# Performance work log

Hardware: AMD Instinct MI355X
Metric: run time of the kernel (lower is better)

The kernel has to match this reference:

```python
import math
import jax, jax.numpy as jnp
import numpy as np

B, L, DM = 2, 1024, 1024
STATE, EXPAND, CONV, DTR = 16, 2, 4, 8
INNER = DM * EXPAND          # 2048
NFFT = L // 2 + 1            # 513


def _silu(v):
    return v * jax.nn.sigmoid(v)


def setup_inputs() -> dict:
    key = jax.random.key(0)
    ks = jax.random.split(key, 12)
    s = lambda k, shape, sc=0.02: (jax.random.normal(k, shape, jnp.float32) * sc)
    # dt_proj bias initialized like the torch module: exp(U(0,1)*(log dt_max - log dt_min) + log dt_min)
    inv_dt = jnp.exp(jax.random.uniform(ks[10], (INNER,), jnp.float32)
                     * (math.log(0.1) - math.log(0.001)) + math.log(0.001))
    return {
        "x": jax.random.normal(ks[0], (B, L, DM), jnp.float32),
        "in_proj_w": s(ks[1], (2 * INNER, DM)),
        "conv_w": s(ks[2], (INNER, 1, CONV), 0.1),      # depthwise conv kernel
        "conv_b": jnp.zeros((INNER,), jnp.float32),
        "A_log": jnp.tile(jnp.log(jnp.arange(1, STATE + 1, dtype=jnp.float32)), (INNER, 1)),
        "D": jnp.ones((INNER,), jnp.float32),
        "x_proj_w": s(ks[3], (DTR + 2 * STATE, INNER)),
        "dt_proj_w": s(ks[4], (INNER, DTR)),
        "dt_proj_b": inv_dt,
        "filter_real": s(ks[5], (INNER, NFFT)),
        "filter_imag": s(ks[6], (INNER, NFFT)),
        "spectral_decay": jnp.ones((INNER,), jnp.float32) * 0.01,
        "fusion_w": s(ks[7], (INNER, 2 * INNER)),
        "fusion_b": jnp.zeros((INNER,), jnp.float32),
        "out_proj_w": s(ks[8], (DM, INNER)),
        "ln_gamma": jnp.ones((DM,), jnp.float32),
        "ln_beta": jnp.zeros((DM,), jnp.float32),
    }


def reference(x, in_proj_w, conv_w, conv_b, A_log, D, x_proj_w, dt_proj_w, dt_proj_b,
              filter_real, filter_imag, spectral_decay, fusion_w, fusion_b,
              out_proj_w, ln_gamma, ln_beta):
    residual = x
    xz = x @ in_proj_w.T                                   # [B,L,2*INNER]
    x_inner, z = xz[..., :INNER], xz[..., INNER:]
    z = _silu(z)

    # ---- SSM path ----
    xc = jnp.swapaxes(x_inner, 1, 2)                       # [B,E,L]
    xc = jax.lax.conv_general_dilated(
        xc, conv_w, (1,), [(CONV - 1, 0)],                 # causal depthwise conv (pad-left == torch pad + truncate)
        dimension_numbers=("NCH", "OIH", "NCH"),
        feature_group_count=INNER) + conv_b[None, :, None]
    x_conv = jnp.swapaxes(_silu(xc), 1, 2)                 # [B,L,E]

    x_dbc = x_conv @ x_proj_w.T                            # [B,L,DTR+2S]
    dt_x = x_dbc[..., :DTR]
    Bm = x_dbc[..., DTR:DTR + STATE]                       # [B,L,S]
    Cm = x_dbc[..., DTR + STATE:]                          # [B,L,S]
    dt = jax.nn.softplus(dt_x @ dt_proj_w.T + dt_proj_b)   # [B,L,E]
    A = -jnp.exp(A_log)                                    # [E,S]
    dA = jnp.exp(dt[..., None] * A)                        # [B,L,E,S]
    dBx = (dt * x_conv)[..., None] * Bm[:, :, None, :]     # [B,L,E,S]

    def step(h, inp):
        dA_t, dBx_t, C_t = inp
        h = dA_t * h + dBx_t                               # [B,E,S]
        return h, jnp.einsum('bes,bs->be', h, C_t)

    h0 = jnp.zeros((B, INNER, STATE), x.dtype)
    _, ys = jax.lax.scan(step, h0,
                         (jnp.swapaxes(dA, 0, 1), jnp.swapaxes(dBx, 0, 1), jnp.swapaxes(Cm, 0, 1)))
    y_ssm = jnp.swapaxes(ys, 0, 1) + x_conv * D            # [B,L,E]

    # ---- Spectral path ----
    xf = jnp.fft.rfft(jnp.swapaxes(x_inner, 1, 2), axis=-1)        # [B,E,NFFT]
    freqs = jnp.linspace(0.0, 1.0, NFFT)
    filt = (filter_real + 1j * filter_imag) * jnp.exp(-spectral_decay[:, None] * freqs[None, :])
    y_spec = jnp.swapaxes(jnp.fft.irfft(xf * filt[None], n=L, axis=-1), 1, 2)  # [B,L,E]

    # ---- Gated fusion ----
    g = jax.nn.sigmoid(jnp.concatenate([y_ssm, y_spec], -1) @ fusion_w.T + fusion_b)
    y = g * y_ssm + (1.0 - g) * y_spec
    y = y * z
    out = y @ out_proj_w.T + residual                      # [B,L,DM]

    mu = out.mean(-1, keepdims=True)
    var = out.var(-1, keepdims=True)
    return (out - mu) / jnp.sqrt(var + 1e-5) * ln_gamma + ln_beta
```

## Files before the change

kernel.cpp:

```cpp
#include <hip/hip_runtime.h>
#include <math.h>

#define B_ 2
#define L_ 1024
#define DM_ 1024
#define STATE_ 16
#define CONV_ 4
#define DTR_ 8
#define INNER_ 2048
#define M_ (B_*L_)
#define MD_ (B_*INNER_)
#define NFFT_ 513
#define NFP_ 1152
#define NCH_ 32
#define CHL_ 32
#define SK_ 32
#define KSL_ (2048/SK_)

typedef unsigned short u16;
typedef __attribute__((ext_vector_type(8))) short short8;
typedef __attribute__((ext_vector_type(8))) __bf16 bf16x8;
typedef __attribute__((ext_vector_type(4))) float f32x4;

__device__ __forceinline__ float frcp_(float x) { return __builtin_amdgcn_rcpf(x); }
__device__ __forceinline__ float fexp_(float x) { return __expf(x); }
__device__ __forceinline__ float fsigm_(float x) { return frcp_(1.f + __expf(-x)); }
__device__ __forceinline__ float fsilu_(float x) { return x * frcp_(1.f + __expf(-x)); }
__device__ __forceinline__ float fsoftplus_(float v) {
  return (v > 20.f) ? v : __logf(1.f + __expf(v));
}
__device__ __forceinline__ u16 f2bf(float f) {
  union { float f; unsigned u; } v; v.f = f;
  unsigned r = v.u + 0x7fffu + ((v.u >> 16) & 1u);
  return (u16)(r >> 16);
}
__device__ __forceinline__ float bf2f(u16 h) {
  union { unsigned u; float f; } v; v.u = ((unsigned)h) << 16;
  return v.f;
}
__device__ __forceinline__ void gload16(const void* g, void* l) {
  __builtin_amdgcn_global_load_lds(
      (const __attribute__((address_space(1))) unsigned*)g,
      (__attribute__((address_space(3))) unsigned*)l, 16, 0, 0);
}
__device__ __forceinline__ f32x4 mfma_bf16(short8 a, short8 b, f32x4 c) {
  return __builtin_amdgcn_mfma_f32_16x16x32_bf16(
      __builtin_bit_cast(bf16x8, a), __builtin_bit_cast(bf16x8, b), c, 0, 0, 0);
}

#define CVT_N0 2097152
#define CVT_N1 6291456
#define CVT_N2 14680064
#define CVT_NT 16777216
__global__ __launch_bounds__(256) void cvt4_k(
    const float* __restrict__ s0, const float* __restrict__ s1,
    const float* __restrict__ s2, const float* __restrict__ s3,
    u16* __restrict__ out)
{
  int i = (blockIdx.x*256 + threadIdx.x) * 4;
  const float* src; int off;
  if (i < CVT_N0)      { src = s0; off = 0; }
  else if (i < CVT_N1) { src = s1; off = CVT_N0; }
  else if (i < CVT_N2) { src = s2; off = CVT_N1; }
  else                 { src = s3; off = CVT_N2; }
  float4 v = *(const float4*)(src + (i - off));
  ushort4 o;
  o.x = f2bf(v.x); o.y = f2bf(v.y); o.z = f2bf(v.z); o.w = f2bf(v.w);
  *(ushort4*)(out + i) = o;
}

template<int TM, int TN, int EPI>
__global__ __launch_bounds__((TM/64)*(TN/32)*64) void mgemm_k(
    const u16* __restrict__ Ab, const u16* __restrict__ Bb,
    void* __restrict__ Cout, int K, int ldc,
    const float* __restrict__ aux0, u16* __restrict__ aux1,
    const float* __restrict__ aux2, const float* __restrict__ aux3)
{
  constexpr int WN   = TN/32;
  constexpr int NW   = (TM/64)*WN;
  constexpr int NTHR = NW*64;
  __shared__ __align__(16) u16 As[2][TM*64];
  __shared__ __align__(16) u16 Bs[2][TN*64];
  const int t = threadIdx.x;
  const int lane = t & 63;
  const int w = t >> 6;
  const int wm = w / WN, wn = w % WN;
  const int M0 = blockIdx.y * TM, N0 = blockIdx.x * TN;

  f32x4 acc[4][2] = {};

  auto stage = [&](int buf, int k0) {
    #pragma unroll
    for (int q = 0; q < TM*8/NTHR; q++) {
      int u = q*NTHR + t;
      int row = u >> 3, gpr = u & 7;
      int grp = gpr ^ (row & 7);
      gload16(Ab + (size_t)(M0+row)*K + k0 + grp*8, &As[buf][u*8]);
    }
    #pragma unroll
    for (int q = 0; q < TN*8/NTHR; q++) {
      int u = q*NTHR + t;
      int row = u >> 3, gpr = u & 7;
      int grp = gpr ^ (row & 7);
      gload16(Bb + (size_t)(N0+row)*K + k0 + grp*8, &Bs[buf][u*8]);
    }
  };

  stage(0, 0);
  const int nk = K >> 6;
  for (int ks = 0; ks < nk; ks++) {
    const int buf = ks & 1;
    __syncthreads();
    if (ks + 1 < nk) stage(buf ^ 1, (ks + 1) << 6);
    const u16* Asb = As[buf];
    const u16* Bsb = Bs[buf];
    #pragma unroll
    for (int kk = 0; kk < 2; kk++) {
      const int quad = lane >> 4;
      const int grp = kk*4 + quad;
      short8 af[4], bf[2];
      #pragma unroll
      for (int i = 0; i < 4; i++) {
        int row = wm*64 + i*16 + (lane & 15);
        af[i] = *(const short8*)&Asb[(row*8 + (grp ^ (row & 7)))*8];
      }
      #pragma unroll
      for (int j = 0; j < 2; j++) {
        int row = wn*32 + j*16 + (lane & 15);
        bf[j] = *(const short8*)&Bsb[(row*8 + (grp ^ (row & 7)))*8];
      }
      #pragma unroll
      for (int i = 0; i < 4; i++)
        #pragma unroll
        for (int j = 0; j < 2; j++)
          acc[i][j] = mfma_bf16(af[i], bf[j], acc[i][j]);
    }
  }

  #pragma unroll
  for (int i = 0; i < 4; i++) {
    int mbase = M0 + wm*64 + i*16 + (lane >> 4)*4;
    #pragma unroll
    for (int j = 0; j < 2; j++) {
      int n = N0 + wn*32 + j*16 + (lane & 15);
      #pragma unroll
      for (int r = 0; r < 4; r++) {
        int m = mbase + r;
        float v = acc[i][j][r];
        if (EPI == 0) {
          ((float*)Cout)[(size_t)m*ldc + n] = v;
        } else if (EPI == 1) {
          float g  = fsigm_(v + aux0[n]);
          float ys = bf2f(aux1[(size_t)m*4096 + n]);
          float yp = bf2f(aux1[(size_t)m*4096 + 2048 + n]);
          float z  = aux2[(size_t)m*4096 + 2048 + n];
          ((u16*)Cout)[(size_t)m*ldc + n] = f2bf((g*ys + (1.f-g)*yp)*fsilu_(z));
        } else if (EPI == 2) {
          ((float*)Cout)[(size_t)m*ldc + n] = v + aux2[(size_t)m*ldc + n];
        } else if (EPI == 3) {
          float pv = __shfl_xor(v, 1, 64);
          int f = n >> 1;
          float outv = 0.f;
          if (f < NFFT_) {
            int c = m & (INNER_-1);
            float d  = fexp_(-aux2[c] * (float)f * (1.f/512.f));
            float wr = aux0[c*NFFT_+f]*d, wi = aux3[c*NFFT_+f]*d;
            float a = (n & 1) ? pv : v;
            float b = (n & 1) ? v : pv;
            outv = (n & 1) ? (a*wi + b*wr) : (a*wr - b*wi);
          }
          ((u16*)Cout)[(size_t)m*ldc + n] = f2bf(outv);
        } else if (EPI == 5) {
          ((float*)Cout)[(size_t)m*ldc + n] = v;
          if (n < 2048) {
            int b2 = m >> 10, l2 = m & 1023;
            aux1[((size_t)(b2*2048 + n) << 10) + l2] = f2bf(v);
          }
        } else {
          int b2 = m >> 11, c2 = m & (INNER_-1);
          ((u16*)Cout)[((size_t)((b2 << 10) + n) << 12) + 2048 + c2] = f2bf(v);
        }
      }
    }
  }
}

__global__ __launch_bounds__(256) void xproj_k(
    const float* __restrict__ xconv, const float* __restrict__ W,
    float* __restrict__ part)
{
  __shared__ float Bs[40][KSL_+4];
  const int sk = blockIdx.x, mt = blockIdx.y;
  const int k0 = sk*KSL_;
  for (int i = threadIdx.x; i < 40*KSL_; i += 256) {
    int n = i >> 6, k = i & (KSL_-1);
    Bs[n][k] = W[(size_t)n*2048 + k0 + k];
  }
  __syncthreads();
  const int m = mt*256 + threadIdx.x;
  const float* arow = xconv + (size_t)m*2048 + k0;
  float acc[40];
  #pragma unroll
  for (int j=0;j<40;j++) acc[j]=0.f;
  for (int k = 0; k < KSL_; k += 4) {
    float4 a = *(const float4*)(arow + k);
    #pragma unroll
    for (int j = 0; j < 40; j++) {
      float4 b = *(const float4*)&Bs[j][k];
      acc[j] += a.x*b.x + a.y*b.y + a.z*b.z + a.w*b.w;
    }
  }
  float* o = part + ((size_t)sk*M_ + m)*40;
  #pragma unroll
  for (int j = 0; j < 10; j++)
    *(float4*)(o + j*4) = make_float4(acc[j*4], acc[j*4+1], acc[j*4+2], acc[j*4+3]);
}

__global__ __launch_bounds__(256) void xpred_k(const float* __restrict__ part,
                                               float* __restrict__ xdbc)
{
  int i = blockIdx.x*256 + threadIdx.x;
  float s = 0.f;
  #pragma unroll
  for (int sk = 0; sk < SK_; sk++) s += part[(size_t)sk*81920 + i];
  xdbc[i] = s;
}

__global__ __launch_bounds__(256) void conv_silu_k(
    const float* __restrict__ xz, const float* __restrict__ cw,
    const float* __restrict__ cb, float* __restrict__ xc)
{
  int idx = blockIdx.x*256 + threadIdx.x;
  int c = idx & (INNER_-1);
  int g = idx >> 11;
  int b = g >> 7;
  int lb = (g & 127) * 8;
  float w0=cw[c*4+0], w1=cw[c*4+1], w2=cw[c*4+2], w3=cw[c*4+3];
  float bias = cb[c];
  float v[11];
  #pragma unroll
  for (int j = 0; j < 11; j++) {
    int l = lb - 3 + j;
    v[j] = (l >= 0) ? xz[((size_t)((b << 10) + l))*4096 + c] : 0.f;
  }
  #pragma unroll
  for (int j = 0; j < 8; j++) {
    float s = bias + w0*v[j] + w1*v[j+1] + w2*v[j+2] + w3*v[j+3];
    xc[((size_t)((b << 10) + lb + j))*INNER_ + c] = fsilu_(s);
  }
}

__global__ __launch_bounds__(256) void scan1_k(
    const float* __restrict__ xdbc, const float* __restrict__ xconv,
    const float* __restrict__ A_log, const float* __restrict__ dtw,
    const float* __restrict__ dtb, float* __restrict__ Pq)
{
  int idx = blockIdx.x*256 + threadIdx.x;
  int e  = idx & (INNER_-1);
  int bc = idx >> 11;
  int ch = bc & (NCH_-1);
  int b  = bc >> 5;
  float A[STATE_];
  #pragma unroll
  for (int s=0;s<STATE_;s++) A[s] = -fexp_(A_log[e*STATE_+s]);
  float w[DTR_];
  #pragma unroll
  for (int r=0;r<DTR_;r++) w[r] = dtw[e*DTR_+r];
  float bias = dtb[e];
  float h[STATE_] = {};
  float sdt = 0.f;
  int mbase = b*L_ + ch*CHL_;
  float dtx[DTR_], Bv[STATE_], xcv;
  {
    const float* row = xdbc + (size_t)mbase*40;
    #pragma unroll
    for (int r=0;r<DTR_;r++) dtx[r] = row[r];
    #pragma unroll
    for (int s=0;s<STATE_;s++) Bv[s] = row[8+s];
    xcv = xconv[(size_t)mbase*INNER_ + e];
  }
  for (int l=0;l<CHL_;l++) {
    float ndtx[DTR_], nBv[STATE_], nxcv = 0.f;
    if (l+1 < CHL_) {
      const float* nrow = xdbc + (size_t)(mbase+l+1)*40;
      #pragma unroll
      for (int r=0;r<DTR_;r++) ndtx[r] = nrow[r];
      #pragma unroll
      for (int s=0;s<STATE_;s++) nBv[s] = nrow[8+s];
      nxcv = xconv[(size_t)(mbase+l+1)*INNER_ + e];
    } else {
      #pragma unroll
      for (int r=0;r<DTR_;r++) ndtx[r] = 0.f;
      #pragma unroll
      for (int s=0;s<STATE_;s++) nBv[s] = 0.f;
    }
    float v = bias;
    #pragma unroll
    for (int r=0;r<DTR_;r++) v += dtx[r]*w[r];
    float dt = fsoftplus_(v);
    sdt += dt;
    float dx = dt * xcv;
    #pragma unroll
    for (int s=0;s<STATE_;s++) {
      float dA = fexp_(dt*A[s]);
      h[s] = dA*h[s] + dx*Bv[s];
    }
    #pragma unroll
    for (int r=0;r<DTR_;r++) dtx[r] = ndtx[r];
    #pragma unroll
    for (int s=0;s<STATE_;s++) Bv[s] = nBv[s];
    xcv = nxcv;
  }
  float* o = Pq + (size_t)idx*32;
  #pragma unroll
  for (int s=0;s<STATE_;s++) { o[s] = fexp_(A[s]*sdt); o[16+s] = h[s]; }
}

__global__ __launch_bounds__(256) void scan2_k(float* __restrict__ Pq)
{
  int idx = blockIdx.x*256 + threadIdx.x;
  int s = idx & 15;
  int e = (idx >> 4) & (INNER_-1);
  int b = idx >> 15;
  float h = 0.f;
  for (int ch = 0; ch < NCH_; ch++) {
    size_t base = ((size_t)(b*NCH_+ch)*INNER_ + e)*32;
    float p = Pq[base + s];
    float q = Pq[base + 16 + s];
    Pq[base + 16 + s] = h;
    h = p*h + q;
  }
}

__global__ __launch_bounds__(256) void scan3_k(
    const float* __restrict__ xdbc, const float* __restrict__ xconv,
    const float* __restrict__ A_log, const float* __restrict__ dtw,
    const float* __restrict__ dtb, const float* __restrict__ Dp,
    const float* __restrict__ Pq, u16* __restrict__ ycat)
{
  int idx = blockIdx.x*256 + threadIdx.x;
  int e  = idx & (INNER_-1);
  int bc = idx >> 11;
  int ch = bc & (NCH_-1);
  int b  = bc >> 5;
  float A[STATE_];
  #pragma unroll
  for (int s=0;s<STATE_;s++) A[s] = -fexp_(A_log[e*STATE_+s]);
  float w[DTR_];
  #pragma unroll
  for (int r=0;r<DTR_;r++) w[r] = dtw[e*DTR_+r];
  float bias = dtb[e];
  float Dv = Dp[e];
  float h[STATE_];
  const float* hi = Pq + (size_t)idx*32 + 16;
  #pragma unroll
  for (int s=0;s<STATE_;s++) h[s] = hi[s];
  int mbase = b*L_ + ch*CHL_;
  float dtx[DTR_], Bv[STATE_], Cv[STATE_], xcv;
  {
    const float* row = xdbc + (size_t)mbase*40;
    #pragma unroll
    for (int r=0;r<DTR_;r++) dtx[r] = row[r];
    #pragma unroll
    for (int s=0;s<STATE_;s++) { Bv[s] = row[8+s]; Cv[s] = row[24+s]; }
    xcv = xconv[(size_t)mbase*INNER_ + e];
  }
  for (int l=0;l<CHL_;l++) {
    float ndtx[DTR_], nBv[STATE_], nCv[STATE_], nxcv = 0.f;
    if (l+1 < CHL_) {
      const float* nrow = xdbc + (size_t)(mbase+l+1)*40;
      #pragma unroll
      for (int r=0;r<DTR_;r++) ndtx[r] = nrow[r];
      #pragma unroll
      for (int s=0;s<STATE_;s++) { nBv[s] = nrow[8+s]; nCv[s] = nrow[24+s]; }
      nxcv = xconv[(size_t)(mbase+l+1)*INNER_ + e];
    } else {
      #pragma unroll
      for (int r=0;r<DTR_;r++) ndtx[r] = 0.f;
      #pragma unroll
      for (int s=0;s<STATE_;s++) { nBv[s] = 0.f; nCv[s] = 0.f; }
    }
    float v = bias;
    #pragma unroll
    for (int r=0;r<DTR_;r++) v += dtx[r]*w[r];
    float dt = fsoftplus_(v);
    float dx = dt * xcv;
    float y = 0.f;
    #pragma unroll
    for (int s=0;s<STATE_;s++) {
      float dA = fexp_(dt*A[s]);
      h[s] = dA*h[s] + dx*Bv[s];
      y += h[s]*Cv[s];
    }
    ycat[(size_t)(mbase+l)*4096 + e] = f2bf(y + xcv*Dv);
    #pragma unroll
    for (int r=0;r<DTR_;r++) dtx[r] = ndtx[r];
    #pragma unroll
    for (int s=0;s<STATE_;s++) { Bv[s] = nBv[s]; Cv[s] = nCv[s]; }
    xcv = nxcv;
  }
}

__global__ __launch_bounds__(256) void genWdftb_k(u16* __restrict__ W) {
  int idx = blockIdx.x*256 + threadIdx.x;
  int l = idx & (L_-1);
  int col = idx >> 10;
  float v = 0.f;
  int f = col >> 1;
  if (f < NFFT_) {
    int ph = (l*f) & (L_-1);
    float th = (float)ph * (6.283185307179586f / (float)L_);
    v = (col & 1) ? -__sinf(th) : __cosf(th);
  }
  W[idx] = f2bf(v);
}

__global__ __launch_bounds__(256) void genWinvb_k(u16* __restrict__ W) {
  int idx = blockIdx.x*256 + threadIdx.x;
  int r = idx % NFP_;
  int l = idx / NFP_;
  int f = r >> 1;
  float v = 0.f;
  if (f < NFFT_) {
    bool edge = (f == 0) || (f == 512);
    float sc = (edge ? 1.f : 2.f) / (float)L_;
    int ph = (f*l) & (L_-1);
    float th = (float)ph * (6.283185307179586f / (float)L_);
    if (r & 1) v = edge ? 0.f : -sc*__sinf(th);
    else       v = sc*__cosf(th);
  }
  W[idx] = f2bf(v);
}

__global__ __launch_bounds__(256) void ln_k(const float* __restrict__ inp,
    const float* __restrict__ gma, const float* __restrict__ bta,
    float* __restrict__ out)
{
  int m = blockIdx.x;
  const float* row = inp + (size_t)m*DM_;
  float s=0.f, s2=0.f;
  float v[4];
  #pragma unroll
  for (int j=0;j<4;j++) {
    v[j] = row[threadIdx.x + j*256];
    s += v[j]; s2 += v[j]*v[j];
  }
  #pragma unroll
  for (int off=32; off>=1; off>>=1) {
    s  += __shfl_down(s, off);
    s2 += __shfl_down(s2, off);
  }
  __shared__ float rs[4], rs2[4], stats[2];
  int wid = threadIdx.x >> 6;
  if ((threadIdx.x & 63) == 0) { rs[wid]=s; rs2[wid]=s2; }
  __syncthreads();
  if (threadIdx.x == 0) {
    float ts  = rs[0]+rs[1]+rs[2]+rs[3];
    float ts2 = rs2[0]+rs2[1]+rs2[2]+rs2[3];
    float mu  = ts/(float)DM_;
    float var = ts2/(float)DM_ - mu*mu;
    stats[0] = mu; stats[1] = rsqrtf(var + 1e-5f);
  }
  __syncthreads();
  float mu = stats[0], rstd = stats[1];
  #pragma unroll
  for (int j=0;j<4;j++) {
    int n = threadIdx.x + j*256;
    out[(size_t)m*DM_ + n] = (v[j]-mu)*rstd*gma[n] + bta[n];
  }
}

extern "C" void kernel_launch(void* const* d_in, const int* in_sizes, int n_in,
                              void* d_out, int out_size, void* d_ws, size_t ws_size,
                              hipStream_t stream)
{
  const float* x       = (const float*)d_in[0];
  const float* in_w    = (const float*)d_in[1];
  const float* conv_w  = (const float*)d_in[2];
  const float* conv_b  = (const float*)d_in[3];
  const float* A_log   = (const float*)d_in[4];
  const float* Dp      = (const float*)d_in[5];
  const float* xproj_w = (const float*)d_in[6];
  const float* dt_w    = (const float*)d_in[7];
  const float* dt_b    = (const float*)d_in[8];
  const float* f_re    = (const float*)d_in[9];
  const float* f_im    = (const float*)d_in[10];
  const float* s_dec   = (const float*)d_in[11];
  const float* fus_w   = (const float*)d_in[12];
  const float* fus_b   = (const float*)d_in[13];
  const float* out_w   = (const float*)d_in[14];
  const float* ln_g    = (const float*)d_in[15];
  const float* ln_b    = (const float*)d_in[16];
  float* out = (float*)d_out;

  float* ws    = (float*)d_ws;
  float* xz    = ws;
  float* xconv = xz    + 8388608;
  float* xdbc  = xconv + 4194304;
  float* Pq    = xdbc  + 81920;
  u16* ub      = (u16*)(Pq + 4194304);
  u16* xb      = ub;
  u16* inwb    = xb    + 2097152;
  u16* fuswb   = inwb  + 4194304;
  u16* outwb   = fuswb + 8388608;
  u16* xt      = outwb + 2097152;
  u16* Wb      = xt    + 4194304;
  u16* XFb     = Wb    + 1179648;
  u16* ycat    = XFb   + 4718592;
  u16* ycomb   = xt;
  float* outp  = xconv;
  float* part  = (float*)ycat;

  cvt4_k<<<CVT_NT/1024, 256, 0, stream>>>(x, in_w, fus_w, out_w, xb);

  mgemm_k<128,128,5><<<dim3(4096/128, M_/128), 512, 0, stream>>>(
      xb, inwb, xz, 1024, 4096, nullptr, xt, nullptr, nullptr);
  conv_silu_k<<<(M_*INNER_/8)/256, 256, 0, stream>>>(xz, conv_w, conv_b, xconv);
  xproj_k<<<dim3(SK_, M_/256), 256, 0, stream>>>(xconv, xproj_w, part);
  xpred_k<<<(M_*40)/256, 256, 0, stream>>>(part, xdbc);
  scan1_k<<<(B_*NCH_*INNER_)/256, 256, 0, stream>>>(xdbc, xconv, A_log, dt_w, dt_b, Pq);
  scan2_k<<<(B_*INNER_*STATE_)/256, 256, 0, stream>>>(Pq);
  scan3_k<<<(B_*NCH_*INNER_)/256, 256, 0, stream>>>(xdbc, xconv, A_log, dt_w, dt_b, Dp, Pq, ycat);
  genWdftb_k<<<(NFP_*1024)/256, 256, 0, stream>>>(Wb);
  mgemm_k<128,64,3><<<dim3(NFP_/64, MD_/128), 256, 0, stream>>>(
      xt, Wb, XFb, 1024, NFP_, f_re, nullptr, s_dec, f_im);
  genWinvb_k<<<(NFP_*1024)/256, 256, 0, stream>>>(Wb);
  mgemm_k<128,64,6><<<dim3(1024/64, MD_/128), 256, 0, stream>>>(
      XFb, Wb, ycat, NFP_, 0, nullptr, nullptr, nullptr, nullptr);
  mgemm_k<128,64,1><<<dim3(2048/64, M_/128), 256, 0, stream>>>(
      ycat, fuswb, ycomb, 4096, 2048, fus_b, ycat, xz, nullptr);
  mgemm_k<64,64,2><<<dim3(1024/64, M_/64), 128, 0, stream>>>(
      ycomb, outwb, outp, 2048, 1024, nullptr, nullptr, x, nullptr);
  ln_k<<<M_, 256, 0, stream>>>(outp, ln_g, ln_b, out);
}
```

Baseline: 410.5 us.

## Enlarge per-warp GEMM tiles, shorten scan chunks, recompute chunk decay in scan2

The GEMM kernel now gives each wavefront a 64x64 output tile (4x4 MFMA accumulators) instead of 64x32, which halves the threads per block and raises register use in exchange for more reuse of A fragments. An explicit lda parameter is added. The chunked SSM scan switches from 32 chunks of length 32 to 64 chunks of length 16. This doubles parallelism in scan1 and scan3 but lengthens the sequential scan2 loop. scan1 now stores only the summed dt per chunk rather than 16 decay products, and scan2 recomputes exp(A*sdt), which cuts scan buffer traffic and reorders the workspace layout.

Result: slower. 445.2 us (+8.5%).

```diff
diff --git a/kernel.cpp b/kernel.cpp
--- a/kernel.cpp
+++ b/kernel.cpp
@@ -12,8 +12,8 @@
 #define MD_ (B_*INNER_)
 #define NFFT_ 513
 #define NFP_ 1152
-#define NCH_ 32
-#define CHL_ 32
+#define NCH_ 64
+#define CHL_ 16
 #define SK_ 32
 #define KSL_ (2048/SK_)
 
@@ -70,13 +70,13 @@
 }
 
 template<int TM, int TN, int EPI>
-__global__ __launch_bounds__((TM/64)*(TN/32)*64) void mgemm_k(
+__global__ __launch_bounds__((TM/64)*(TN/64)*64) void mgemm_k(
     const u16* __restrict__ Ab, const u16* __restrict__ Bb,
-    void* __restrict__ Cout, int K, int ldc,
+    void* __restrict__ Cout, int K, int lda, int ldc,
     const float* __restrict__ aux0, u16* __restrict__ aux1,
     const float* __restrict__ aux2, const float* __restrict__ aux3)
 {
-  constexpr int WN   = TN/32;
+  constexpr int WN   = TN/64;
   constexpr int NW   = (TM/64)*WN;
   constexpr int NTHR = NW*64;
   __shared__ __align__(16) u16 As[2][TM*64];
@@ -87,7 +87,7 @@
   const int wm = w / WN, wn = w % WN;
   const int M0 = blockIdx.y * TM, N0 = blockIdx.x * TN;
 
-  f32x4 acc[4][2] = {};
+  f32x4 acc[4][4] = {};
 
   auto stage = [&](int buf, int k0) {
     #pragma unroll
@@ -95,14 +95,14 @@
       int u = q*NTHR + t;
       int row = u >> 3, gpr = u & 7;
       int grp = gpr ^ (row & 7);
-      gload16(Ab + (size_t)(M0+row)*K + k0 + grp*8, &As[buf][u*8]);
+      gload16(Ab + (size_t)(M0+row)*lda + k0 + grp*8, &As[buf][u*8]);
     }
     #pragma unroll
     for (int q = 0; q < TN*8/NTHR; q++) {
       int u = q*NTHR + t;
       int row = u >> 3, gpr = u & 7;
       int grp = gpr ^ (row & 7);
-      gload16(Bb + (size_t)(N0+row)*K + k0 + grp*8, &Bs[buf][u*8]);
+      gload16(Bb + (size_t)(N0+row)*lda + k0 + grp*8, &Bs[buf][u*8]);
     }
   };
 
@@ -118,21 +118,21 @@
     for (int kk = 0; kk < 2; kk++) {
       const int quad = lane >> 4;
       const int grp = kk*4 + quad;
-      short8 af[4], bf[2];
+      short8 af[4], bf[4];
       #pragma unroll
       for (int i = 0; i < 4; i++) {
         int row = wm*64 + i*16 + (lane & 15);
         af[i] = *(const short8*)&Asb[(row*8 + (grp ^ (row & 7)))*8];
       }
       #pragma unroll
-      for (int j = 0; j < 2; j++) {
-        int row = wn*32 + j*16 + (lane & 15);
+      for (int j = 0; j < 4; j++) {
+        int row = wn*64 + j*16 + (lane & 15);
         bf[j] = *(const short8*)&Bsb[(row*8 + (grp ^ (row & 7)))*8];
       }
       #pragma unroll
       for (int i = 0; i < 4; i++)
         #pragma unroll
-        for (int j = 0; j < 2; j++)
+        for (int j = 0; j < 4; j++)
           acc[i][j] = mfma_bf16(af[i], bf[j], acc[i][j]);
     }
   }
@@ -141,8 +141,8 @@
   for (int i = 0; i < 4; i++) {
     int mbase = M0 + wm*64 + i*16 + (lane >> 4)*4;
     #pragma unroll
-    for (int j = 0; j < 2; j++) {
-      int n = N0 + wn*32 + j*16 + (lane & 15);
+    for (int j = 0; j < 4; j++) {
+      int n = N0 + wn*64 + j*16 + (lane & 15);
       #pragma unroll
       for (int r = 0; r < 4; r++) {
         int m = mbase + r;
@@ -253,13 +253,14 @@
 __global__ __launch_bounds__(256) void scan1_k(
     const float* __restrict__ xdbc, const float* __restrict__ xconv,
     const float* __restrict__ A_log, const float* __restrict__ dtw,
-    const float* __restrict__ dtb, float* __restrict__ Pq)
+    const float* __restrict__ dtb, float* __restrict__ qbuf,
+    float* __restrict__ sdtb)
 {
   int idx = blockIdx.x*256 + threadIdx.x;
   int e  = idx & (INNER_-1);
   int bc = idx >> 11;
   int ch = bc & (NCH_-1);
-  int b  = bc >> 5;
+  int b  = bc >> 6;
   float A[STATE_];
   #pragma unroll
   for (int s=0;s<STATE_;s++) A[s] = -fexp_(A_log[e*STATE_+s]);
@@ -311,23 +312,27 @@
     for (int s=0;s<STATE_;s++) Bv[s] = nBv[s];
     xcv = nxcv;
   }
-  float* o = Pq + (size_t)idx*32;
-  #pragma unroll
-  for (int s=0;s<STATE_;s++) { o[s] = fexp_(A[s]*sdt); o[16+s] = h[s]; }
-}
-
-__global__ __launch_bounds__(256) void scan2_k(float* __restrict__ Pq)
+  sdtb[idx] = sdt;
+  float* o = qbuf + (size_t)idx*16;
+  #pragma unroll
+  for (int s=0;s<STATE_;s++) o[s] = h[s];
+}
+
+__global__ __launch_bounds__(256) void scan2_k(float* __restrict__ qbuf,
+                                               const float* __restrict__ sdtb,
+                                               const float* __restrict__ A_log)
 {
   int idx = blockIdx.x*256 + threadIdx.x;
   int s = idx & 15;
   int e = (idx >> 4) & (INNER_-1);
   int b = idx >> 15;
+  float As = -fexp_(A_log[e*STATE_+s]);
   float h = 0.f;
   for (int ch = 0; ch < NCH_; ch++) {
-    size_t base = ((size_t)(b*NCH_+ch)*INNER_ + e)*32;
-    float p = Pq[base + s];
-    float q = Pq[base + 16 + s];
-    Pq[base + 16 + s] = h;
+    size_t tix = ((size_t)(b*NCH_+ch)*INNER_ + e);
+    float p = fexp_(As * sdtb[tix]);
+    float q = qbuf[tix*16 + s];
+    qbuf[tix*16 + s] = h;
     h = p*h + q;
   }
 }
@@ -336,13 +341,13 @@
     const float* __restrict__ xdbc, const float* __restrict__ xconv,
     const float* __restrict__ A_log, const float* __restrict__ dtw,
     const float* __restrict__ dtb, const float* __restrict__ Dp,
-    const float* __restrict__ Pq, u16* __restrict__ ycat)
+    const float* __restrict__ qbuf, u16* __restrict__ ycat)
 {
   int idx = blockIdx.x*256 + threadIdx.x;
   int e  = idx & (INNER_-1);
   int bc = idx >> 11;
   int ch = bc & (NCH_-1);
-  int b  = bc >> 5;
+  int b  = bc >> 6;
   float A[STATE_];
   #pragma unroll
   for (int s=0;s<STATE_;s++) A[s] = -fexp_(A_log[e*STATE_+s]);
@@ -352,7 +357,7 @@
   float bias = dtb[e];
   float Dv = Dp[e];
   float h[STATE_];
-  const float* hi = Pq + (size_t)idx*32 + 16;
+  const float* hi = qbuf + (size_t)idx*16;
   #pragma unroll
   for (int s=0;s<STATE_;s++) h[s] = hi[s];
   int mbase = b*L_ + ch*CHL_;
@@ -495,10 +500,10 @@
 
   float* ws    = (float*)d_ws;
   float* xz    = ws;
-  float* xconv = xz    + 8388608;
-  float* xdbc  = xconv + 4194304;
-  float* Pq    = xdbc  + 81920;
-  u16* ub      = (u16*)(Pq + 4194304);
+  float* xdbc  = xz    + 8388608;
+  float* xconv = xdbc  + 81920;
+  float* qbuf  = xconv + 4194304;
+  u16* ub      = (u16*)(qbuf + 4194304);
   u16* xb      = ub;
   u16* inwb    = xb    + 2097152;
   u16* fuswb   = inwb  + 4194304;
@@ -509,27 +514,28 @@
   u16* ycat    = XFb   + 4718592;
   u16* ycomb   = xt;
   float* outp  = xconv;
+  float* sdtb  = (float*)Wb;
   float* part  = (float*)ycat;
 
   cvt4_k<<<CVT_NT/1024, 256, 0, stream>>>(x, in_w, fus_w, out_w, xb);
 
-  mgemm_k<128,128,5><<<dim3(4096/128, M_/128), 512, 0, stream>>>(
-      xb, inwb, xz, 1024, 4096, nullptr, xt, nullptr, nullptr);
+  mgemm_k<128,128,5><<<dim3(4096/128, M_/128), 256, 0, stream>>>(
+      xb, inwb, xz, 1024, 1024, 4096, nullptr, xt, nullptr, nullptr);
   conv_silu_k<<<(M_*INNER_/8)/256, 256, 0, stream>>>(xz, conv_w, conv_b, xconv);
   xproj_k<<<dim3(SK_, M_/256), 256, 0, stream>>>(xconv, xproj_w, part);
   xpred_k<<<(M_*40)/256, 256, 0, stream>>>(part, xdbc);
-  scan1_k<<<(B_*NCH_*INNER_)/256, 256, 0, stream>>>(xdbc, xconv, A_log, dt_w, dt_b, Pq);
-  scan2_k<<<(B_*INNER_*STATE_)/256, 256, 0, stream>>>(Pq);
-  scan3_k<<<(B_*NCH_*INNER_)/256, 256, 0, stream>>>(xdbc, xconv, A_log, dt_w, dt_b, Dp, Pq, ycat);
+  scan1_k<<<(B_*NCH_*INNER_)/256, 256, 0, stream>>>(xdbc, xconv, A_log, dt_w, dt_b, qbuf, sdtb);
+  scan2_k<<<(B_*INNER_*STATE_)/256, 256, 0, stream>>>(qbuf, sdtb, A_log);
+  scan3_k<<<(B_*NCH_*INNER_)/256, 256, 0, stream>>>(xdbc, xconv, A_log, dt_w, dt_b, Dp, qbuf, ycat);
   genWdftb_k<<<(NFP_*1024)/256, 256, 0, stream>>>(Wb);
-  mgemm_k<128,64,3><<<dim3(NFP_/64, MD_/128), 256, 0, stream>>>(
-      xt, Wb, XFb, 1024, NFP_, f_re, nullptr, s_dec, f_im);
+  mgemm_k<128,64,3><<<dim3(NFP_/64, MD_/128), 128, 0, stream>>>(
+      xt, Wb, XFb, 1024, 1024, NFP_, f_re, nullptr, s_dec, f_im);
   genWinvb_k<<<(NFP_*1024)/256, 256, 0, stream>>>(Wb);
-  mgemm_k<128,64,6><<<dim3(1024/64, MD_/128), 256, 0, stream>>>(
-      XFb, Wb, ycat, NFP_, 0, nullptr, nullptr, nullptr, nullptr);
-  mgemm_k<128,64,1><<<dim3(2048/64, M_/128), 256, 0, stream>>>(
-      ycat, fuswb, ycomb, 4096, 2048, fus_b, ycat, xz, nullptr);
-  mgemm_k<64,64,2><<<dim3(1024/64, M_/64), 128, 0, stream>>>(
-      ycomb, outwb, outp, 2048, 1024, nullptr, nullptr, x, nullptr);
+  mgemm_k<128,64,6><<<dim3(1024/64, MD_/128), 128, 0, stream>>>(
+      XFb, Wb, ycat, NFP_, NFP_, 0, nullptr, nullptr, nullptr, nullptr);
+  mgemm_k<128,64,1><<<dim3(2048/64, M_/128), 128, 0, stream>>>(
+      ycat, fuswb, ycomb, 4096, 4096, 2048, fus_b, ycat, xz, nullptr);
+  mgemm_k<64,64,2><<<dim3(1024/64, M_/64), 64, 0, stream>>>(
+      ycomb, outwb, outp, 2048, 2048, 1024, nullptr, nullptr, x, nullptr);
   ln_k<<<M_, 256, 0, stream>>>(outp, ln_g, ln_b, out);
 }
```
